# Kernel optimization log

Measured on AMD Instinct MI355X. Metric: run time of the kernel, lower is better.

## Reference

```python
import jax, jax.numpy as jnp
import numpy as np

B, N, F_IN = 32, 1024, 64   # batch, num_nodes, diffusion_size[0]
K = 3                        # expansion_step
H = 2                        # num_heads
HID, RAW, OUT, CLS = 128, 128, 128, 2
D1, D2 = 128, 128            # diffusion_size[1], diffusion_size[2]
CAT = D1 + RAW               # concat dim fed to attention (h || h_prime) = 256


def setup_inputs() -> dict:
    key = jax.random.key(0)
    ks = jax.random.split(key, 40)
    g = lambda i, shape: jax.random.normal(ks[i], shape, dtype=jnp.float32) * 0.05
    inp = {
        'X': jax.random.normal(ks[0], (B, N, F_IN), dtype=jnp.float32),
        'A': jax.random.uniform(ks[1], (B, N, N), dtype=jnp.float32),
        # transition tensors / mixing weights (only the 2 layers used in forward)
        'T': g(2, (2, K, N, N)),
        'theta': jnp.full((2, K), 1.0 / K, dtype=jnp.float32),
        # raw feature projection
        'W_raw': g(3, (F_IN, RAW)), 'b_raw': jnp.zeros((RAW,), jnp.float32),
        # diffusion layer linears
        'Wd0': g(4, (F_IN, D1)), 'bd0': jnp.zeros((D1,), jnp.float32),
        'Wd1': g(5, (D1, D2)),   'bd1': jnp.zeros((D2,), jnp.float32),
        # final classifier
        'W_fin': g(6, (OUT, CLS)), 'b_fin': jnp.zeros((CLS,), jnp.float32),
    }
    # two CatMultiAttn blocks: q/k/v projections (CAT->HID), out proj (HID->OUT)
    i = 7
    for l in range(2):
        for nm in ('q', 'k', 'v'):
            inp[f'W{nm}{l}'] = g(i, (CAT, HID)); i += 1
            inp[f'b{nm}{l}'] = jnp.zeros((HID,), jnp.float32)
        inp[f'Wo{l}'] = g(i, (HID, OUT)); i += 1
        inp[f'bo{l}'] = jnp.zeros((OUT,), jnp.float32)
    return inp


def _diffusion(theta_l, T_l, h, A, W, b):
    # Q = sum_k theta_k * T_k  (generalized graph diffusion transition)
    Q = jnp.einsum('k,kij->ij', theta_l, T_l)          # [N,N]
    S = Q[None, :, :] * A                               # [B,N,N] mask by adjacency
    z = jnp.einsum('bij,bjf->bif', S, h)                # diffuse features
    return jax.nn.relu(z @ W + b)


def _cat_attn(h, hp, Wq, bq, Wk, bk, Wv, bv, Wo, bo):
    # concatenate diffused + embedding features, multi-head self-attn over nodes
    x = jnp.concatenate([h, hp], axis=-1)               # [B,N,CAT]
    b, n, _ = x.shape
    q = (x @ Wq + bq).reshape(b, n, H, HID // H)
    k = (x @ Wk + bk).reshape(b, n, H, HID // H)
    v = (x @ Wv + bv).reshape(b, n, H, HID // H)
    scale = jnp.asarray(1.0 / np.sqrt(HID // H), x.dtype)
    s = jnp.einsum('bnhd,bmhd->bhnm', q, k) * scale     # [B,H,N,N]
    p = jax.nn.softmax(s, axis=-1)
    ctx = jnp.einsum('bhnm,bmhd->bnhd', p, v).reshape(b, n, HID)
    return jax.nn.relu(ctx @ Wo + bo)


def reference(X, A, T, theta, W_raw, b_raw, Wd0, bd0, Wd1, bd1,
              W_fin, b_fin,
              Wq0, bq0, Wk0, bk0, Wv0, bv0, Wo0, bo0,
              Wq1, bq1, Wk1, bk1, Wv1, bv1, Wo1, bo1):
    theta_soft = jax.nn.softmax(theta, axis=-1)         # [2,K]
    h_prime = X @ W_raw + b_raw                          # [B,N,RAW]
    # layer 0
    h = _diffusion(theta_soft[0], T[0], X, A, Wd0, bd0)  # [B,N,D1]
    h_prime = _cat_attn(h, h_prime, Wq0, bq0, Wk0, bk0, Wv0, bv0, Wo0, bo0)
    # layer 1 (residual fusion)
    h = _diffusion(theta_soft[1], T[1], h, A, Wd1, bd1)  # [B,N,D2]
    h_prime = h_prime + _cat_attn(h, h_prime, Wq1, bq1, Wk1, bk1, Wv1, bv1, Wo1, bo1)
    return h_prime @ W_fin + b_fin                       # [B,N,CLS]
```

## Files before the change

### kernel.cpp

```cpp
#include <hip/hip_runtime.h>
#include <hip/hip_bf16.h>

typedef __hip_bfloat16 bf16;
typedef __attribute__((ext_vector_type(8))) short s8b;
typedef __attribute__((ext_vector_type(4))) short s4b;
typedef __attribute__((ext_vector_type(4))) float f4;

#define BB   32
#define NN   1024
#define FIN  64
#define HEADS 2
#define DH   64
#define HIDD 128
#define SZQ  ((size_t)BB * NN * HIDD)

__device__ __forceinline__ ushort f2bf(float x) {
    bf16 h = __float2bfloat16(x);
    return *(ushort*)&h;
}
__device__ __forceinline__ float bfbits2f(ushort h) {
    union { uint u; float f; } c; c.u = (uint)h << 16; return c.f;
}
__device__ __forceinline__ uint pk_bf16(float lo, float hi) {
    return (uint)f2bf(lo) | ((uint)f2bf(hi) << 16);
}
union U8 { short s[8]; s8b v; };
union U4 { short s[4]; s4b v; };
union UQ { ushort u[8]; s8b v; };

__global__ __launch_bounds__(256) void build_q_split_kernel(const float* __restrict__ T,
                                                            const float* __restrict__ theta,
                                                            int layer,
                                                            ushort* __restrict__ Qhi,
                                                            ushort* __restrict__ Qlo) {
    float t0 = theta[layer * 3 + 0];
    float t1 = theta[layer * 3 + 1];
    float t2 = theta[layer * 3 + 2];
    float m  = fmaxf(t0, fmaxf(t1, t2));
    float e0 = expf(t0 - m), e1 = expf(t1 - m), e2 = expf(t2 - m);
    float inv = 1.0f / (e0 + e1 + e2);
    e0 *= inv; e1 *= inv; e2 *= inv;
    size_t base = ((size_t)blockIdx.x * 256 + threadIdx.x) * 8;
    const float* Tl = T + (size_t)layer * 3 * NN * NN;
    U8 hi, lo;
#pragma unroll
    for (int i = 0; i < 8; i++) {
        float q = e0 * Tl[base + i]
                + e1 * Tl[base + i + (size_t)NN * NN]
                + e2 * Tl[base + i + (size_t)2 * NN * NN];
        ushort hh = f2bf(q);
        hi.s[i] = (short)hh;
        lo.s[i] = (short)f2bf(q - bfbits2f(hh));
    }
    *(s8b*)&Qhi[base] = hi.v;
    *(s8b*)&Qlo[base] = lo.v;
}

__global__ __launch_bounds__(256) void prep_w_kernel(
        const float* __restrict__ raw, const float* __restrict__ d0,
        const float* __restrict__ d1,
        const float* __restrict__ q0, const float* __restrict__ k0,
        const float* __restrict__ v0, const float* __restrict__ o0,
        const float* __restrict__ q1, const float* __restrict__ k1,
        const float* __restrict__ v1, const float* __restrict__ o1,
        ushort* __restrict__ hi, ushort* __restrict__ lo) {
    int id = blockIdx.x * 256 + threadIdx.x;
    const float* src; int K, off;
    if      (id <   8192) { src = raw; K =  64; off = 0; }
    else if (id <  16384) { src = d0;  K =  64; off = 8192; }
    else if (id <  32768) { src = d1;  K = 128; off = 16384; }
    else if (id <  65536) { src = q0;  K = 256; off = 32768; }
    else if (id <  98304) { src = k0;  K = 256; off = 65536; }
    else if (id < 131072) { src = v0;  K = 256; off = 98304; }
    else if (id < 147456) { src = o0;  K = 128; off = 131072; }
    else if (id < 180224) { src = q1;  K = 256; off = 147456; }
    else if (id < 212992) { src = k1;  K = 256; off = 180224; }
    else if (id < 245760) { src = v1;  K = 256; off = 212992; }
    else                  { src = o1;  K = 128; off = 245760; }
    int il = id - off;
    int k = il >> 7, c = il & 127;
    float w = src[il];
    ushort h = f2bf(w);
    hi[off + c * K + k] = h;
    lo[off + c * K + k] = f2bf(w - bfbits2f(h));
}

__global__ __launch_bounds__(256) void transpose_split64_kernel(const float* __restrict__ X,
                                                                ushort* __restrict__ hiT,
                                                                ushort* __restrict__ loT) {
    __shared__ float tile[64][65];
    const int b  = blockIdx.x >> 4;
    const int n0 = (blockIdx.x & 15) * 64;
    const int t  = threadIdx.x;
    {
        int nl = t >> 2, f0 = (t & 3) * 16;
        const float* xp = X + ((size_t)b * NN + n0 + nl) * 64 + f0;
#pragma unroll
        for (int i = 0; i < 16; i += 4)
            *(float4*)&tile[nl][f0 + i] = *(const float4*)(xp + i);
    }
    __syncthreads();
    {
        int f = t >> 2, n1 = (t & 3) * 16;
        U8 h0, h1, l0, l1;
#pragma unroll
        for (int i = 0; i < 16; i++) {
            float v = tile[n1 + i][f];
            ushort hh = f2bf(v);
            ushort ll = f2bf(v - bfbits2f(hh));
            if (i < 8) { h0.s[i] = (short)hh; l0.s[i] = (short)ll; }
            else       { h1.s[i - 8] = (short)hh; l1.s[i - 8] = (short)ll; }
        }
        size_t gb = ((size_t)b * 64 + f) * NN + n0 + n1;
        *(s8b*)&hiT[gb]     = h0.v;  *(s8b*)&hiT[gb + 8] = h1.v;
        *(s8b*)&loT[gb]     = l0.v;  *(s8b*)&loT[gb + 8] = l1.v;
    }
}

template<int F>
__global__ __launch_bounds__(512, 4) void diffusion_mfma_kernel(
        const ushort* __restrict__ Qhi, const ushort* __restrict__ Qlo,
        const float* __restrict__ A,
        const ushort* __restrict__ hT_hi, const ushort* __restrict__ hT_lo,
        float* __restrict__ z) {
    constexpr int SS  = 72;
    constexpr int NT  = F / 16;
    constexpr int TPW = NT / 2;
    __shared__ short Shi[64][SS], Slo[64][SS];
    __shared__ short Hhi[F][SS],  Hlo[F][SS];

    const int b  = blockIdx.x >> 4;
    const int i0 = (blockIdx.x & 15) * 64;
    const int t  = threadIdx.x;
    const int w  = t >> 6, lane = t & 63;
    const int quad = lane >> 4, c = lane & 15;
    const int mt = w >> 1, nh = w & 1;

    const int srow = t >> 3, scol = (t & 7) * 8;
    const float*  Ap = A   + ((size_t)b * NN + i0 + srow) * NN + scol;
    const ushort* Qh = Qhi + (size_t)(i0 + srow) * NN + scol;
    const ushort* Ql = Qlo + (size_t)(i0 + srow) * NN + scol;
    constexpr int HTR = 512 / F;
    constexpr int HJ  = 64 / HTR;
    constexpr int HV  = HJ / 8;
    const int hrow = t / HTR, hcol = (t % HTR) * HJ;
    const ushort* Hh = hT_hi + ((size_t)b * F + hrow) * NN + hcol;
    const ushort* Hl = hT_lo + ((size_t)b * F + hrow) * NN + hcol;

    f4 acc[TPW];
#pragma unroll
    for (int i = 0; i < TPW; i++) acc[i] = (f4){0.f, 0.f, 0.f, 0.f};

    float4 a0 = *(const float4*)Ap, a1 = *(const float4*)(Ap + 4);
    s8b hhv[HV], hlv[HV];
#pragma unroll
    for (int vv = 0; vv < HV; vv++) {
        hhv[vv] = *(const s8b*)(Hh + 8 * vv);
        hlv[vv] = *(const s8b*)(Hl + 8 * vv);
    }

#pragma unroll 1
    for (int j0 = 0; j0 < NN; j0 += 64) {
        UQ qh, ql;
        qh.v = *(const s8b*)(Qh + j0);
        ql.v = *(const s8b*)(Ql + j0);
        __syncthreads();
        {
            float av[8] = {a0.x, a0.y, a0.z, a0.w, a1.x, a1.y, a1.z, a1.w};
            U8 hi, lo;
#pragma unroll
            for (int i = 0; i < 8; i++) {
                float q = bfbits2f(qh.u[i]) + bfbits2f(ql.u[i]);
                float s = q * av[i];
                ushort hb = f2bf(s);
                hi.s[i] = (short)hb;
                lo.s[i] = (short)f2bf(s - bfbits2f(hb));
            }
            *(s8b*)&Shi[srow][scol] = hi.v;
            *(s8b*)&Slo[srow][scol] = lo.v;
#pragma unroll
            for (int vv = 0; vv < HV; vv++) {
                *(s8b*)&Hhi[hrow][hcol + 8 * vv] = hhv[vv];
                *(s8b*)&Hlo[hrow][hcol + 8 * vv] = hlv[vv];
            }
        }
        if (j0 + 64 < NN) {
            a0 = *(const float4*)(Ap + j0 + 64);
            a1 = *(const float4*)(Ap + j0 + 68);
#pragma unroll
            for (int vv = 0; vv < HV; vv++) {
                hhv[vv] = *(const s8b*)(Hh + j0 + 64 + 8 * vv);
                hlv[vv] = *(const s8b*)(Hl + j0 + 64 + 8 * vv);
            }
        }
        __syncthreads();

#pragma unroll
        for (int ks = 0; ks < 2; ks++) {
            s8b ahi = *(const s8b*)&Shi[mt * 16 + c][ks * 32 + quad * 8];
            s8b alo = *(const s8b*)&Slo[mt * 16 + c][ks * 32 + quad * 8];
#pragma unroll
            for (int tt = 0; tt < TPW; tt++) {
                const int nt = nh * TPW + tt;
                s8b bhi = *(const s8b*)&Hhi[nt * 16 + c][ks * 32 + quad * 8];
                s8b blo = *(const s8b*)&Hlo[nt * 16 + c][ks * 32 + quad * 8];
                acc[tt] = __builtin_amdgcn_mfma_f32_16x16x32_bf16(ahi, bhi, acc[tt], 0, 0, 0);
                acc[tt] = __builtin_amdgcn_mfma_f32_16x16x32_bf16(alo, bhi, acc[tt], 0, 0, 0);
                acc[tt] = __builtin_amdgcn_mfma_f32_16x16x32_bf16(ahi, blo, acc[tt], 0, 0, 0);
            }
        }
    }
#pragma unroll
    for (int tt = 0; tt < TPW; tt++)
#pragma unroll
        for (int r = 0; r < 4; r++)
            z[((size_t)b * NN + i0 + mt * 16 + quad * 4 + r) * F + (nh * TPW + tt) * 16 + c] = acc[tt][r];
}

template<int K1, int K2, int CB, bool RELU, bool RESID, int OMODE>
__global__ __launch_bounds__(256) void dense_mfma_kernel(
        const float* __restrict__ in1, const float* __restrict__ in2,
        const ushort* __restrict__ WT_hi, const ushort* __restrict__ WT_lo,
        const float* __restrict__ bias, const float* __restrict__ biask,
        const float* __restrict__ biasv,
        float* __restrict__ out, ushort* __restrict__ outq,
        ushort* __restrict__ hiT, ushort* __restrict__ loT) {
    constexpr int KD  = K1 + K2;
    constexpr int NKT = KD / 32;
    constexpr int NCT = CB / 16;
    __shared__ short Xhi[64][40], Xlo[64][40];
    __shared__ short Whi[CB][40], Wlo[CB][40];

    const int r0 = blockIdx.x * 64;
    const int c0 = blockIdx.y * CB;
    const int t  = threadIdx.x;
    const int w  = t >> 6, lane = t & 63;
    const int quad = lane >> 4, c = lane & 15;

    f4 acc[NCT];
#pragma unroll
    for (int i = 0; i < NCT; i++) acc[i] = (f4){0.f, 0.f, 0.f, 0.f};

    for (int kt = 0; kt < NKT; kt++) {
        const int k0 = kt * 32;
        __syncthreads();
        {
            int row = t >> 2, kk = (t & 3) * 8;
            int g = r0 + row;
            const float* p;
            if (K2 > 0) {
                int k = k0 + kk;
                p = (k < K1) ? (in1 + (size_t)g * K1 + k)
                             : (in2 + (size_t)g * K2 + (k - K1));
            } else {
                p = in1 + (size_t)g * K1 + k0 + kk;
            }
            float4 a = *(const float4*)p, bq = *(const float4*)(p + 4);
            float sv[8] = {a.x, a.y, a.z, a.w, bq.x, bq.y, bq.z, bq.w};
            U8 hi, lo;
#pragma unroll
            for (int i = 0; i < 8; i++) {
                ushort hh = f2bf(sv[i]);
                hi.s[i] = (short)hh;
                lo.s[i] = (short)f2bf(sv[i] - bfbits2f(hh));
            }
            *(s8b*)&Xhi[row][kk] = hi.v;
            *(s8b*)&Xlo[row][kk] = lo.v;
        }
        {
#pragma unroll
            for (int p = 0; p < CB / 64; p++) {
                int cc = p * 64 + (t >> 2), kk = (t & 3) * 8;
                size_t gsrc = (size_t)(c0 + cc) * KD + k0 + kk;
                *(s8b*)&Whi[cc][kk] = *(const s8b*)&WT_hi[gsrc];
                *(s8b*)&Wlo[cc][kk] = *(const s8b*)&WT_lo[gsrc];
            }
        }
        __syncthreads();

        s8b ah = *(const s8b*)&Xhi[16 * w + c][quad * 8];
        s8b al = *(const s8b*)&Xlo[16 * w + c][quad * 8];
#pragma unroll
        for (int ct = 0; ct < NCT; ct++) {
            s8b bh = *(const s8b*)&Whi[ct * 16 + c][quad * 8];
            s8b bl = *(const s8b*)&Wlo[ct * 16 + c][quad * 8];
            acc[ct] = __builtin_amdgcn_mfma_f32_16x16x32_bf16(ah, bh, acc[ct], 0, 0, 0);
            acc[ct] = __builtin_amdgcn_mfma_f32_16x16x32_bf16(al, bh, acc[ct], 0, 0, 0);
            acc[ct] = __builtin_amdgcn_mfma_f32_16x16x32_bf16(ah, bl, acc[ct], 0, 0, 0);
        }
    }

    const int row_g0 = r0 + 16 * w + quad * 4;
#pragma unroll
    for (int ct = 0; ct < NCT; ct++) {
        const int col = c0 + ct * 16 + c;
        if (OMODE == 1) {
            int tensor = col >> 7, cc2 = col & 127;
            float bv = (tensor == 0 ? bias : tensor == 1 ? biask : biasv)[cc2];
            int head = cc2 >> 6, d = cc2 & 63;
            int b = row_g0 >> 10, n = row_g0 & 1023;
            ushort* dst = outq + (size_t)tensor * SZQ
                        + (((size_t)b * HEADS + head) * NN + n) * 64 + d;
#pragma unroll
            for (int r = 0; r < 4; r++) dst[(size_t)r * 64] = f2bf(acc[ct][r] + bv);
        } else {
            float bv = bias[col];
            float vv[4];
#pragma unroll
            for (int r = 0; r < 4; r++) {
                float v = acc[ct][r] + bv;
                if (RELU) v = fmaxf(v, 0.f);
                size_t o = (size_t)(row_g0 + r) * 128 + col;
                if (RESID) v += out[o];
                out[o] = v;
                vv[r] = v;
            }
            if (OMODE == 2) {
                int b = row_g0 >> 10, n = row_g0 & 1023;
                U4 ph, pl;
#pragma unroll
                for (int r = 0; r < 4; r++) {
                    ushort hh = f2bf(vv[r]);
                    ph.s[r] = (short)hh;
                    pl.s[r] = (short)f2bf(vv[r] - bfbits2f(hh));
                }
                size_t tb = ((size_t)b * 128 + col) * NN + n;
                *(s4b*)&hiT[tb] = ph.v;
                *(s4b*)&loT[tb] = pl.v;
            }
        }
    }
}

__global__ __launch_bounds__(256) void attn_mfma_kernel(const ushort* __restrict__ q,
                                                        const ushort* __restrict__ k,
                                                        const ushort* __restrict__ v,
                                                        float* __restrict__ ctx) {
    __shared__ short Ks[64][68];
    __shared__ short Vt[64][68];

    const int bh = blockIdx.x >> 4;
    const int n0 = (blockIdx.x & 15) * 64;
    const int b  = bh >> 1, h = bh & 1;
    const int t  = threadIdx.x;
    const int w  = t >> 6;
    const int lane = t & 63;
    const int quad = lane >> 4, c = lane & 15;
    const size_t kvbase = (size_t)bh * NN * 64;
    const float scale = 0.125f;

    s8b qf0, qf1;
    {
        const ushort* qrow = q + kvbase + (size_t)(n0 + 16 * w + c) * 64;
        qf0 = *(const s8b*)(qrow + quad * 8);
        qf1 = *(const s8b*)(qrow + 32 + quad * 8);
    }

    f4 O[4];
#pragma unroll
    for (int i = 0; i < 4; i++) O[i] = (f4){0.f, 0.f, 0.f, 0.f};
    float m_i = -1e30f, l_i = 0.f;

    for (int kt0 = 0; kt0 < NN; kt0 += 64) {
        __syncthreads();
        {
            int key = t >> 2, d0 = (t & 3) * 16;
            const ushort* kr = k + kvbase + (size_t)(kt0 + key) * 64 + d0;
            s8b k0 = *(const s8b*)kr, k1 = *(const s8b*)(kr + 8);
            *(s4b*)&Ks[key][d0]      = __builtin_shufflevector(k0, k0, 0, 1, 2, 3);
            *(s4b*)&Ks[key][d0 + 4]  = __builtin_shufflevector(k0, k0, 4, 5, 6, 7);
            *(s4b*)&Ks[key][d0 + 8]  = __builtin_shufflevector(k1, k1, 0, 1, 2, 3);
            *(s4b*)&Ks[key][d0 + 12] = __builtin_shufflevector(k1, k1, 4, 5, 6, 7);
            int vkey = t & 63, vd0 = (t >> 6) * 16;
            const ushort* vr = v + kvbase + (size_t)(kt0 + vkey) * 64 + vd0;
            s8b v0 = *(const s8b*)vr, v1 = *(const s8b*)(vr + 8);
#pragma unroll
            for (int i = 0; i < 8; i++) {
                Vt[vd0 + i][vkey]     = v0[i];
                Vt[vd0 + 8 + i][vkey] = v1[i];
            }
        }
        __syncthreads();

#pragma unroll
        for (int u = 0; u < 2; u++) {
            const int kb = u * 32;
            f4 sa = (f4){0.f, 0.f, 0.f, 0.f};
            f4 sb = (f4){0.f, 0.f, 0.f, 0.f};
#pragma unroll
            for (int ch = 0; ch < 2; ch++) {
                const short* pa = &Ks[kb + c][ch * 32 + quad * 8];
                const short* pb = &Ks[kb + 16 + c][ch * 32 + quad * 8];
                s4b a0 = *(const s4b*)pa, a1 = *(const s4b*)(pa + 4);
                s4b b0 = *(const s4b*)pb, b1 = *(const s4b*)(pb + 4);
                s8b ka = __builtin_shufflevector(a0, a1, 0, 1, 2, 3, 4, 5, 6, 7);
                s8b kB = __builtin_shufflevector(b0, b1, 0, 1, 2, 3, 4, 5, 6, 7);
                s8b qf = ch ? qf1 : qf0;
                sa = __builtin_amdgcn_mfma_f32_16x16x32_bf16(ka, qf, sa, 0, 0, 0);
                sb = __builtin_amdgcn_mfma_f32_16x16x32_bf16(kB, qf, sb, 0, 0, 0);
            }
            float pv[8];
#pragma unroll
            for (int r = 0; r < 4; r++) { pv[r] = sa[r] * scale; pv[4 + r] = sb[r] * scale; }
            float mx = pv[0];
#pragma unroll
            for (int j = 1; j < 8; j++) mx = fmaxf(mx, pv[j]);
            mx = fmaxf(mx, __shfl_xor(mx, 16));
            mx = fmaxf(mx, __shfl_xor(mx, 32));
            float newm  = fmaxf(m_i, mx);
            float alpha = __expf(m_i - newm);
            float ps = 0.f;
#pragma unroll
            for (int j = 0; j < 8; j++) { pv[j] = __expf(pv[j] - newm); ps += pv[j]; }
            ps += __shfl_xor(ps, 16);
            ps += __shfl_xor(ps, 32);
            l_i = l_i * alpha + ps;
            m_i = newm;
#pragma unroll
            for (int dt = 0; dt < 4; dt++)
#pragma unroll
                for (int r = 0; r < 4; r++) O[dt][r] *= alpha;

            uint Da01 = pk_bf16(pv[0], pv[1]), Da23 = pk_bf16(pv[2], pv[3]);
            uint Db01 = pk_bf16(pv[4], pv[5]), Db23 = pk_bf16(pv[6], pv[7]);
            int addr0 = ((((2 * quad) & 3) << 4) | c) << 2;
            int addr1 = ((((2 * quad + 1) & 3) << 4) | c) << 2;
            int A01_0 = __builtin_amdgcn_ds_bpermute(addr0, (int)Da01);
            int A23_0 = __builtin_amdgcn_ds_bpermute(addr0, (int)Da23);
            int B01_0 = __builtin_amdgcn_ds_bpermute(addr0, (int)Db01);
            int B23_0 = __builtin_amdgcn_ds_bpermute(addr0, (int)Db23);
            int A01_1 = __builtin_amdgcn_ds_bpermute(addr1, (int)Da01);
            int A23_1 = __builtin_amdgcn_ds_bpermute(addr1, (int)Da23);
            int B01_1 = __builtin_amdgcn_ds_bpermute(addr1, (int)Db01);
            int B23_1 = __builtin_amdgcn_ds_bpermute(addr1, (int)Db23);
            int tsel = quad >> 1;
            union { int i[4]; s8b s; } pf;
            pf.i[0] = tsel ? B01_0 : A01_0;
            pf.i[1] = tsel ? B23_0 : A23_0;
            pf.i[2] = tsel ? B01_1 : A01_1;
            pf.i[3] = tsel ? B23_1 : A23_1;

#pragma unroll
            for (int dt = 0; dt < 4; dt++) {
                const short* pvp = &Vt[16 * dt + c][kb + quad * 8];
                s4b v0 = *(const s4b*)pvp, v1 = *(const s4b*)(pvp + 4);
                s8b vf = __builtin_shufflevector(v0, v1, 0, 1, 2, 3, 4, 5, 6, 7);
                O[dt] = __builtin_amdgcn_mfma_f32_16x16x32_bf16(vf, pf.s, O[dt], 0, 0, 0);
            }
        }
    }

    float inv = 1.0f / l_i;
    float* crow = ctx + ((size_t)b * NN + n0 + 16 * w + c) * HIDD + h * DH;
#pragma unroll
    for (int dt = 0; dt < 4; dt++)
#pragma unroll
        for (int r = 0; r < 4; r++)
            crow[16 * dt + 4 * quad + r] = O[dt][r] * inv;
}

__global__ __launch_bounds__(256) void final_kernel(const float* __restrict__ hp,
                                                    const float* __restrict__ Wf,
                                                    const float* __restrict__ bf_,
                                                    float* __restrict__ out) {
    int id = blockIdx.x * blockDim.x + threadIdx.x;
    int r = id >> 1, c = id & 1;
    const float* row = hp + (size_t)r * 128;
    float acc = bf_[c];
    for (int kk = 0; kk < 128; kk++) acc += row[kk] * Wf[kk * 2 + c];
    out[id] = acc;
}

extern "C" void kernel_launch(void* const* d_in, const int* in_sizes, int n_in,
                              void* d_out, int out_size, void* d_ws, size_t ws_size,
                              hipStream_t stream) {
    (void)in_sizes; (void)n_in; (void)out_size; (void)ws_size;
    const float* X     = (const float*)d_in[0];
    const float* A     = (const float*)d_in[1];
    const float* T     = (const float*)d_in[2];
    const float* theta = (const float*)d_in[3];
    const float* W_raw = (const float*)d_in[4];
    const float* b_raw = (const float*)d_in[5];
    const float* Wd0   = (const float*)d_in[6];
    const float* bd0   = (const float*)d_in[7];
    const float* Wd1   = (const float*)d_in[8];
    const float* bd1   = (const float*)d_in[9];
    const float* W_fin = (const float*)d_in[10];
    const float* b_fin = (const float*)d_in[11];
    const float* Wq0 = (const float*)d_in[12]; const float* bq0 = (const float*)d_in[13];
    const float* Wk0 = (const float*)d_in[14]; const float* bk0 = (const float*)d_in[15];
    const float* Wv0 = (const float*)d_in[16]; const float* bv0 = (const float*)d_in[17];
    const float* Wo0 = (const float*)d_in[18]; const float* bo0 = (const float*)d_in[19];
    const float* Wq1 = (const float*)d_in[20]; const float* bq1 = (const float*)d_in[21];
    const float* Wk1 = (const float*)d_in[22]; const float* bk1 = (const float*)d_in[23];
    const float* Wv1 = (const float*)d_in[24]; const float* bv1 = (const float*)d_in[25];
    const float* Wo1 = (const float*)d_in[26]; const float* bo1 = (const float*)d_in[27];

    float* ws   = (float*)d_ws;
    const size_t SZ = (size_t)BB * NN * HIDD;
    ushort* Qhi = (ushort*)ws;
    ushort* Qlo = Qhi + (size_t)NN * NN;
    float* hp   = ws + (size_t)NN * NN;
    float* h    = hp + SZ;
    float* z    = h + SZ;
    ushort* qb  = (ushort*)(z + SZ);
    ushort* kb  = qb + SZ;
    ushort* vb  = kb + SZ;
    ushort* XT_hi = vb + SZ;
    ushort* XT_lo = XT_hi + SZ / 2;
    ushort* hT_hi = XT_lo + SZ / 2;
    ushort* hT_lo = hT_hi + SZ;
    ushort* WT_hi = hT_lo + SZ;
    ushort* WT_lo = WT_hi + 262144;

    const int OFF_RAW = 0, OFF_D0 = 8192, OFF_D1 = 16384, OFF_QKV0 = 32768,
              OFF_O0 = 131072, OFF_QKV1 = 147456, OFF_O1 = 245760;

    const int attnGrid = BB * HEADS * (NN / 64);
    const int diffGrid = BB * (NN / 64);
    const dim3 dg1(512, 1), dg2(512, 2);

    prep_w_kernel<<<1024, 256, 0, stream>>>(W_raw, Wd0, Wd1, Wq0, Wk0, Wv0, Wo0,
                                            Wq1, Wk1, Wv1, Wo1, WT_hi, WT_lo);
    build_q_split_kernel<<<(NN * NN) / (256 * 8), 256, 0, stream>>>(T, theta, 0, Qhi, Qlo);
    transpose_split64_kernel<<<BB * (NN / 64), 256, 0, stream>>>(X, XT_hi, XT_lo);

    dense_mfma_kernel<64, 0, 128, false, false, 0><<<dg1, 256, 0, stream>>>(
        X, nullptr, WT_hi + OFF_RAW, WT_lo + OFF_RAW, b_raw, nullptr, nullptr,
        hp, nullptr, nullptr, nullptr);
    diffusion_mfma_kernel<64><<<diffGrid, 512, 0, stream>>>(Qhi, Qlo, A, XT_hi, XT_lo, z);
    dense_mfma_kernel<64, 0, 128, true, false, 2><<<dg1, 256, 0, stream>>>(
        z, nullptr, WT_hi + OFF_D0, WT_lo + OFF_D0, bd0, nullptr, nullptr,
        h, nullptr, hT_hi, hT_lo);
    dense_mfma_kernel<128, 128, 192, false, false, 1><<<dg2, 256, 0, stream>>>(
        h, hp, WT_hi + OFF_QKV0, WT_lo + OFF_QKV0, bq0, bk0, bv0,
        nullptr, qb, nullptr, nullptr);
    attn_mfma_kernel<<<attnGrid, 256, 0, stream>>>(qb, kb, vb, z);
    dense_mfma_kernel<128, 0, 128, true, false, 0><<<dg1, 256, 0, stream>>>(
        z, nullptr, WT_hi + OFF_O0, WT_lo + OFF_O0, bo0, nullptr, nullptr,
        hp, nullptr, nullptr, nullptr);

    build_q_split_kernel<<<(NN * NN) / (256 * 8), 256, 0, stream>>>(T, theta, 1, Qhi, Qlo);
    diffusion_mfma_kernel<128><<<diffGrid, 512, 0, stream>>>(Qhi, Qlo, A, hT_hi, hT_lo, z);
    dense_mfma_kernel<128, 0, 128, true, false, 0><<<dg1, 256, 0, stream>>>(
        z, nullptr, WT_hi + OFF_D1, WT_lo + OFF_D1, bd1, nullptr, nullptr,
        h, nullptr, nullptr, nullptr);
    dense_mfma_kernel<128, 128, 192, false, false, 1><<<dg2, 256, 0, stream>>>(
        h, hp, WT_hi + OFF_QKV1, WT_lo + OFF_QKV1, bq1, bk1, bv1,
        nullptr, qb, nullptr, nullptr);
    attn_mfma_kernel<<<attnGrid, 256, 0, stream>>>(qb, kb, vb, z);
    dense_mfma_kernel<128, 0, 128, true, true, 0><<<dg1, 256, 0, stream>>>(
        z, nullptr, WT_hi + OFF_O1, WT_lo + OFF_O1, bo1, nullptr, nullptr,
        hp, nullptr, nullptr, nullptr);

    final_kernel<<<(BB * NN * 2) / 256, 256, 0, stream>>>(hp, W_fin, b_fin, (float*)d_out);
}
```

Measured before the change: 569.9 us.

## Fuse final classifier into output projection and widen attention key tile

Adds an output mode to the dense kernel that applies the residual, multiplies by the 128x2 classifier weights in registers, reduces across lanes, and writes logits directly. This removes the separate final kernel and the write and re-read of hp. The attention kernel now stages 128 keys per iteration instead of 64, halving the barriers and online-softmax rescale steps. The cost is more shared memory and registers per block, which could lower occupancy.

```diff
diff --git a/kernel.cpp b/kernel.cpp
--- a/kernel.cpp
+++ b/kernel.cpp
@@ -224,7 +224,9 @@
         const float* __restrict__ bias, const float* __restrict__ biask,
         const float* __restrict__ biasv,
         float* __restrict__ out, ushort* __restrict__ outq,
-        ushort* __restrict__ hiT, ushort* __restrict__ loT) {
+        ushort* __restrict__ hiT, ushort* __restrict__ loT,
+        const float* __restrict__ Wfin, const float* __restrict__ bfin,
+        float* __restrict__ fout) {
     constexpr int KD  = K1 + K2;
     constexpr int NKT = KD / 32;
     constexpr int NCT = CB / 16;
@@ -291,6 +293,39 @@
     }
 
     const int row_g0 = r0 + 16 * w + quad * 4;
+    if (OMODE == 3) {
+        float fc0[4] = {0.f, 0.f, 0.f, 0.f};
+        float fc1[4] = {0.f, 0.f, 0.f, 0.f};
+#pragma unroll
+        for (int ct = 0; ct < NCT; ct++) {
+            const int col = c0 + ct * 16 + c;
+            float bv = bias[col];
+            float w0 = Wfin[col * 2], w1 = Wfin[col * 2 + 1];
+#pragma unroll
+            for (int r = 0; r < 4; r++) {
+                float v = acc[ct][r] + bv;
+                if (RELU) v = fmaxf(v, 0.f);
+                if (RESID) v += out[(size_t)(row_g0 + r) * 128 + col];
+                fc0[r] += v * w0;
+                fc1[r] += v * w1;
+            }
+        }
+#pragma unroll
+        for (int r = 0; r < 4; r++) {
+            float a0 = fc0[r], a1 = fc1[r];
+#pragma unroll
+            for (int off = 1; off < 16; off <<= 1) {
+                a0 += __shfl_xor(a0, off, 16);
+                a1 += __shfl_xor(a1, off, 16);
+            }
+            if (c == 0) {
+                size_t row = row_g0 + r;
+                fout[row * 2]     = a0 + bfin[0];
+                fout[row * 2 + 1] = a1 + bfin[1];
+            }
+        }
+        return;
+    }
 #pragma unroll
     for (int ct = 0; ct < NCT; ct++) {
         const int col = c0 + ct * 16 + c;
@@ -336,8 +371,8 @@
                                                         const ushort* __restrict__ k,
                                                         const ushort* __restrict__ v,
                                                         float* __restrict__ ctx) {
-    __shared__ short Ks[64][68];
-    __shared__ short Vt[64][68];
+    __shared__ short Ks[128][68];
+    __shared__ short Vt[64][136];
 
     const int bh = blockIdx.x >> 4;
     const int n0 = (blockIdx.x & 15) * 64;
@@ -361,32 +396,34 @@
     for (int i = 0; i < 4; i++) O[i] = (f4){0.f, 0.f, 0.f, 0.f};
     float m_i = -1e30f, l_i = 0.f;
 
-    for (int kt0 = 0; kt0 < NN; kt0 += 64) {
+    for (int kt0 = 0; kt0 < NN; kt0 += 128) {
         __syncthreads();
-        {
+#pragma unroll
+        for (int half = 0; half < 2; half++) {
             int key = t >> 2, d0 = (t & 3) * 16;
-            const ushort* kr = k + kvbase + (size_t)(kt0 + key) * 64 + d0;
+            const ushort* kr = k + kvbase + (size_t)(kt0 + 64 * half + key) * 64 + d0;
             s8b k0 = *(const s8b*)kr, k1 = *(const s8b*)(kr + 8);
-            *(s4b*)&Ks[key][d0]      = __builtin_shufflevector(k0, k0, 0, 1, 2, 3);
-            *(s4b*)&Ks[key][d0 + 4]  = __builtin_shufflevector(k0, k0, 4, 5, 6, 7);
-            *(s4b*)&Ks[key][d0 + 8]  = __builtin_shufflevector(k1, k1, 0, 1, 2, 3);
-            *(s4b*)&Ks[key][d0 + 12] = __builtin_shufflevector(k1, k1, 4, 5, 6, 7);
+            *(s4b*)&Ks[64 * half + key][d0]      = __builtin_shufflevector(k0, k0, 0, 1, 2, 3);
+            *(s4b*)&Ks[64 * half + key][d0 + 4]  = __builtin_shufflevector(k0, k0, 4, 5, 6, 7);
+            *(s4b*)&Ks[64 * half + key][d0 + 8]  = __builtin_shufflevector(k1, k1, 0, 1, 2, 3);
+            *(s4b*)&Ks[64 * half + key][d0 + 12] = __builtin_shufflevector(k1, k1, 4, 5, 6, 7);
             int vkey = t & 63, vd0 = (t >> 6) * 16;
-            const ushort* vr = v + kvbase + (size_t)(kt0 + vkey) * 64 + vd0;
+            const ushort* vr = v + kvbase + (size_t)(kt0 + 64 * half + vkey) * 64 + vd0;
             s8b v0 = *(const s8b*)vr, v1 = *(const s8b*)(vr + 8);
 #pragma unroll
             for (int i = 0; i < 8; i++) {
-                Vt[vd0 + i][vkey]     = v0[i];
-                Vt[vd0 + 8 + i][vkey] = v1[i];
+                Vt[vd0 + i][64 * half + vkey]     = v0[i];
+                Vt[vd0 + 8 + i][64 * half + vkey] = v1[i];
             }
         }
         __syncthreads();
 
-#pragma unroll
-        for (int u = 0; u < 2; u++) {
-            const int kb = u * 32;
-            f4 sa = (f4){0.f, 0.f, 0.f, 0.f};
-            f4 sb = (f4){0.f, 0.f, 0.f, 0.f};
+        f4 sg[4][2];
+#pragma unroll
+        for (int g = 0; g < 4; g++) {
+            const int kb = g * 32;
+            sg[g][0] = (f4){0.f, 0.f, 0.f, 0.f};
+            sg[g][1] = (f4){0.f, 0.f, 0.f, 0.f};
 #pragma unroll
             for (int ch = 0; ch < 2; ch++) {
                 const short* pa = &Ks[kb + c][ch * 32 + quad * 8];
@@ -396,35 +433,49 @@
                 s8b ka = __builtin_shufflevector(a0, a1, 0, 1, 2, 3, 4, 5, 6, 7);
                 s8b kB = __builtin_shufflevector(b0, b1, 0, 1, 2, 3, 4, 5, 6, 7);
                 s8b qf = ch ? qf1 : qf0;
-                sa = __builtin_amdgcn_mfma_f32_16x16x32_bf16(ka, qf, sa, 0, 0, 0);
-                sb = __builtin_amdgcn_mfma_f32_16x16x32_bf16(kB, qf, sb, 0, 0, 0);
-            }
-            float pv[8];
-#pragma unroll
-            for (int r = 0; r < 4; r++) { pv[r] = sa[r] * scale; pv[4 + r] = sb[r] * scale; }
-            float mx = pv[0];
-#pragma unroll
-            for (int j = 1; j < 8; j++) mx = fmaxf(mx, pv[j]);
-            mx = fmaxf(mx, __shfl_xor(mx, 16));
-            mx = fmaxf(mx, __shfl_xor(mx, 32));
-            float newm  = fmaxf(m_i, mx);
-            float alpha = __expf(m_i - newm);
-            float ps = 0.f;
-#pragma unroll
-            for (int j = 0; j < 8; j++) { pv[j] = __expf(pv[j] - newm); ps += pv[j]; }
-            ps += __shfl_xor(ps, 16);
-            ps += __shfl_xor(ps, 32);
-            l_i = l_i * alpha + ps;
-            m_i = newm;
-#pragma unroll
-            for (int dt = 0; dt < 4; dt++)
-#pragma unroll
-                for (int r = 0; r < 4; r++) O[dt][r] *= alpha;
-
-            uint Da01 = pk_bf16(pv[0], pv[1]), Da23 = pk_bf16(pv[2], pv[3]);
-            uint Db01 = pk_bf16(pv[4], pv[5]), Db23 = pk_bf16(pv[6], pv[7]);
-            int addr0 = ((((2 * quad) & 3) << 4) | c) << 2;
-            int addr1 = ((((2 * quad + 1) & 3) << 4) | c) << 2;
+                sg[g][0] = __builtin_amdgcn_mfma_f32_16x16x32_bf16(ka, qf, sg[g][0], 0, 0, 0);
+                sg[g][1] = __builtin_amdgcn_mfma_f32_16x16x32_bf16(kB, qf, sg[g][1], 0, 0, 0);
+            }
+        }
+        float pv[4][8];
+        float mx = -1e30f;
+#pragma unroll
+        for (int g = 0; g < 4; g++)
+#pragma unroll
+            for (int r = 0; r < 4; r++) {
+                pv[g][r]     = sg[g][0][r] * scale;
+                pv[g][4 + r] = sg[g][1][r] * scale;
+                mx = fmaxf(mx, fmaxf(pv[g][r], pv[g][4 + r]));
+            }
+        mx = fmaxf(mx, __shfl_xor(mx, 16));
+        mx = fmaxf(mx, __shfl_xor(mx, 32));
+        float newm  = fmaxf(m_i, mx);
+        float alpha = __expf(m_i - newm);
+        float ps = 0.f;
+#pragma unroll
+        for (int g = 0; g < 4; g++)
+#pragma unroll
+            for (int j = 0; j < 8; j++) {
+                pv[g][j] = __expf(pv[g][j] - newm);
+                ps += pv[g][j];
+            }
+        ps += __shfl_xor(ps, 16);
+        ps += __shfl_xor(ps, 32);
+        l_i = l_i * alpha + ps;
+        m_i = newm;
+#pragma unroll
+        for (int dt = 0; dt < 4; dt++)
+#pragma unroll
+            for (int r = 0; r < 4; r++) O[dt][r] *= alpha;
+
+        int addr0 = ((((2 * quad) & 3) << 4) | c) << 2;
+        int addr1 = ((((2 * quad + 1) & 3) << 4) | c) << 2;
+        int tsel = quad >> 1;
+#pragma unroll
+        for (int g = 0; g < 4; g++) {
+            const int kb = g * 32;
+            uint Da01 = pk_bf16(pv[g][0], pv[g][1]), Da23 = pk_bf16(pv[g][2], pv[g][3]);
+            uint Db01 = pk_bf16(pv[g][4], pv[g][5]), Db23 = pk_bf16(pv[g][6], pv[g][7]);
             int A01_0 = __builtin_amdgcn_ds_bpermute(addr0, (int)Da01);
             int A23_0 = __builtin_amdgcn_ds_bpermute(addr0, (int)Da23);
             int B01_0 = __builtin_amdgcn_ds_bpermute(addr0, (int)Db01);
@@ -433,13 +484,11 @@
             int A23_1 = __builtin_amdgcn_ds_bpermute(addr1, (int)Da23);
             int B01_1 = __builtin_amdgcn_ds_bpermute(addr1, (int)Db01);
             int B23_1 = __builtin_amdgcn_ds_bpermute(addr1, (int)Db23);
-            int tsel = quad >> 1;
             union { int i[4]; s8b s; } pf;
             pf.i[0] = tsel ? B01_0 : A01_0;
             pf.i[1] = tsel ? B23_0 : A23_0;
             pf.i[2] = tsel ? B01_1 : A01_1;
             pf.i[3] = tsel ? B23_1 : A23_1;
-
 #pragma unroll
             for (int dt = 0; dt < 4; dt++) {
                 const short* pvp = &Vt[16 * dt + c][kb + quad * 8];
@@ -457,18 +506,6 @@
 #pragma unroll
         for (int r = 0; r < 4; r++)
             crow[16 * dt + 4 * quad + r] = O[dt][r] * inv;
-}
-
-__global__ __launch_bounds__(256) void final_kernel(const float* __restrict__ hp,
-                                                    const float* __restrict__ Wf,
-                                                    const float* __restrict__ bf_,
-                                                    float* __restrict__ out) {
-    int id = blockIdx.x * blockDim.x + threadIdx.x;
-    int r = id >> 1, c = id & 1;
-    const float* row = hp + (size_t)r * 128;
-    float acc = bf_[c];
-    for (int kk = 0; kk < 128; kk++) acc += row[kk] * Wf[kk * 2 + c];
-    out[id] = acc;
 }
 
 extern "C" void kernel_launch(void* const* d_in, const int* in_sizes, int n_in,
@@ -527,31 +564,29 @@
 
     dense_mfma_kernel<64, 0, 128, false, false, 0><<<dg1, 256, 0, stream>>>(
         X, nullptr, WT_hi + OFF_RAW, WT_lo + OFF_RAW, b_raw, nullptr, nullptr,
-        hp, nullptr, nullptr, nullptr);
+        hp, nullptr, nullptr, nullptr, nullptr, nullptr, nullptr);
     diffusion_mfma_kernel<64><<<diffGrid, 512, 0, stream>>>(Qhi, Qlo, A, XT_hi, XT_lo, z);
     dense_mfma_kernel<64, 0, 128, true, false, 2><<<dg1, 256, 0, stream>>>(
         z, nullptr, WT_hi + OFF_D0, WT_lo + OFF_D0, bd0, nullptr, nullptr,
-        h, nullptr, hT_hi, hT_lo);
+        h, nullptr, hT_hi, hT_lo, nullptr, nullptr, nullptr);
     dense_mfma_kernel<128, 128, 192, false, false, 1><<<dg2, 256, 0, stream>>>(
         h, hp, WT_hi + OFF_QKV0, WT_lo + OFF_QKV0, bq0, bk0, bv0,
-        nullptr, qb, nullptr, nullptr);
+        nullptr, qb, nullptr, nullptr, nullptr, nullptr, nullptr);
     attn_mfma_kernel<<<attnGrid, 256, 0, stream>>>(qb, kb, vb, z);
     dense_mfma_kernel<128, 0, 128, true, false, 0><<<dg1, 256, 0, stream>>>(
         z, nullptr, WT_hi + OFF_O0, WT_lo + OFF_O0, bo0, nullptr, nullptr,
-        hp, nullptr, nullptr, nullptr);
+        hp, nullptr, nullptr, nullptr, nullptr, nullptr, nullptr);
 
     build_q_split_kernel<<<(NN * NN) / (256 * 8), 256, 0, stream>>>(T, theta, 1, Qhi, Qlo);
     diffusion_mfma_kernel<128><<<diffGrid, 512, 0, stream>>>(Qhi, Qlo, A, hT_hi, hT_lo, z);
     dense_mfma_kernel<128, 0, 128, true, false, 0><<<dg1, 256, 0, stream>>>(
         z, nullptr, WT_hi + OFF_D1, WT_lo + OFF_D1, bd1, nullptr, nullptr,
-        h, nullptr, nullptr, nullptr);
+        h, nullptr, nullptr, nullptr, nullptr, nullptr, nullptr);
     dense_mfma_kernel<128, 128, 192, false, false, 1><<<dg2, 256, 0, stream>>>(
         h, hp, WT_hi + OFF_QKV1, WT_lo + OFF_QKV1, bq1, bk1, bv1,
-        nullptr, qb, nullptr, nullptr);
+        nullptr, qb, nullptr, nullptr, nullptr, nullptr, nullptr);
     attn_mfma_kernel<<<attnGrid, 256, 0, stream>>>(qb, kb, vb, z);
-    dense_mfma_kernel<128, 0, 128, true, true, 0><<<dg1, 256, 0, stream>>>(
+    dense_mfma_kernel<128, 0, 128, true, true, 3><<<dg1, 256, 0, stream>>>(
         z, nullptr, WT_hi + OFF_O1, WT_lo + OFF_O1, bo1, nullptr, nullptr,
-        hp, nullptr, nullptr, nullptr);
-
-    final_kernel<<<(BB * NN * 2) / 256, 256, 0, stream>>>(hp, W_fin, b_fin, (float*)d_out);
-}
+        hp, nullptr, nullptr, nullptr, W_fin, b_fin, (float*)d_out);
+}
```

New measurement: 539.4 us. -5.3%, faster.
